# Kernel tuning notes

Measured on AMD Instinct MI355X. Metric: run time of the kernel, lower is better.

Reference implementation:

```python
import jax, jax.numpy as jnp
import numpy as np

D_MODEL = 1024
N_HEADS = 16
HEAD_DIM = D_MODEL // N_HEADS
EPS = 1e-6


def setup_inputs() -> dict:
    key = jax.random.key(0)
    ks = jax.random.split(key, 10)
    s = 0.02
    return {
        "sequence": jax.random.normal(ks[0], (4, 2048, D_MODEL), dtype=jnp.float32),
        "ln_gamma": jnp.ones((D_MODEL,), jnp.float32),
        "ln_beta": jnp.zeros((D_MODEL,), jnp.float32),
        "Wq": jax.random.normal(ks[1], (D_MODEL, D_MODEL), jnp.float32) * s,
        "bq": jnp.zeros((D_MODEL,), jnp.float32),
        "Wk": jax.random.normal(ks[2], (D_MODEL, D_MODEL), jnp.float32) * s,
        "bk": jnp.zeros((D_MODEL,), jnp.float32),
        "Wv": jax.random.normal(ks[3], (D_MODEL, D_MODEL), jnp.float32) * s,
        "bv": jnp.zeros((D_MODEL,), jnp.float32),
        "Wo": jax.random.normal(ks[4], (D_MODEL, D_MODEL), jnp.float32) * s,
        "bo": jnp.zeros((D_MODEL,), jnp.float32),
        "mu": jnp.zeros((1, 1, 1, 1), jnp.float32),
    }


def _split_heads(x):
    b, s, d = x.shape
    return x.reshape(b, s, N_HEADS, HEAD_DIM).transpose(0, 2, 1, 3)  # [B,H,S,hd]


def reference(sequence, ln_gamma, ln_beta, Wq, bq, Wk, bk, Wv, bv, Wo, bo, mu):
    # LayerNorm (eps=1e-6)
    mean = jnp.mean(sequence, axis=-1, keepdims=True)
    var = jnp.mean(jnp.square(sequence - mean), axis=-1, keepdims=True)
    x = (sequence - mean) / jnp.sqrt(var + EPS) * ln_gamma + ln_beta

    # QKV projections (torch Linear: x @ W.T + b)
    q = _split_heads(x @ Wq.T + bq)
    k = _split_heads(x @ Wk.T + bk)
    v = _split_heads(x @ Wv.T + bv)

    scale = HEAD_DIM ** 0.5
    scores = jnp.einsum("bhqd,bhkd->bhqk", q, k) / scale  # [B,H,S,S]
    scores = jax.nn.sigmoid(scores - mu) * jnp.exp(scores)
    scores = scores / jnp.sum(scores, axis=-1, keepdims=True)

    out = jnp.einsum("bhqk,bhkd->bhqd", scores, v)  # [B,H,S,hd]
    b, h, s, hd = out.shape
    out = out.transpose(0, 2, 1, 3).reshape(b, s, h * hd)
    return out @ Wo.T + bo  # dropout is identity at inference
```

## Files before the change

kernel.cpp:

```cpp
#include <hip/hip_runtime.h>
#include <hip/hip_bf16.h>
#include <cstdint>
#include <cstddef>


typedef __bf16 bf16_t;
typedef __bf16 bf16x4 __attribute__((ext_vector_type(4)));
typedef __bf16 bf16x8 __attribute__((ext_vector_type(8)));
typedef float  f32x4  __attribute__((ext_vector_type(4)));
typedef float  f32x16 __attribute__((ext_vector_type(16)));
typedef unsigned u32x4 __attribute__((ext_vector_type(4)));

#define MFMA16(a, b, c) __builtin_amdgcn_mfma_f32_16x16x32_bf16((a), (b), (c), 0, 0, 0)
#define MFMA32(a, b, c) __builtin_amdgcn_mfma_f32_32x32x16_bf16((a), (b), (c), 0, 0, 0)

#if __has_builtin(__builtin_amdgcn_exp2f)
#define VEXP2(x) __builtin_amdgcn_exp2f(x)
#else
#define VEXP2(x) __expf((x) * 0.6931471805599453f)
#endif

__device__ __forceinline__ unsigned cvtpk_bf16(float a, float b) {
  unsigned r;
  asm("v_cvt_pk_bf16_f32 %0, %1, %2" : "=v"(r) : "v"(a), "v"(b));
  return r;
}

__device__ __forceinline__ void plane32_swap(unsigned& a, unsigned& b) {
  asm volatile("v_permlane32_swap_b32 %0, %1" : "+v"(a), "+v"(b));
}

__device__ __forceinline__ void gload16(void* lds, const void* g) {
  __builtin_amdgcn_global_load_lds(
      (__attribute__((address_space(1))) void*)(uintptr_t)g,
      (__attribute__((address_space(3))) void*)(uint32_t)(uintptr_t)lds,
      16, 0, 0);
}

__global__ __launch_bounds__(256) void prep_k(
    const float* __restrict__ s0, const float* __restrict__ s1,
    const float* __restrict__ s2, const float* __restrict__ s3,
    bf16_t* __restrict__ wdst,
    const float* __restrict__ x, const float* __restrict__ gamma,
    const float* __restrict__ beta, bf16_t* __restrict__ xout)
{
  int bid = blockIdx.x;
  int tid = threadIdx.x;
  if (bid < 4096) {
    int part = bid >> 10;
    const float* src = part == 0 ? s0 : part == 1 ? s1 : part == 2 ? s2 : s3;
    int i = (bid & 1023) * 256 + tid;
    float4 v = ((const float4*)src)[i];
    bf16x4 o = { (bf16_t)v.x, (bf16_t)v.y, (bf16_t)v.z, (bf16_t)v.w };
    *(bf16x4*)(wdst + (((size_t)part) << 20) + (size_t)i * 4) = o;
  } else {
    int row = bid - 4096;
    float4 v = ((const float4*)(x + (size_t)row * 1024))[tid];
    float s  = v.x + v.y + v.z + v.w;
    float ss = v.x * v.x + v.y * v.y + v.z * v.z + v.w * v.w;
#pragma unroll
    for (int m = 1; m < 64; m <<= 1) { s += __shfl_xor(s, m); ss += __shfl_xor(ss, m); }
    __shared__ float sh_s[4], sh_q[4];
    int w = tid >> 6;
    if ((tid & 63) == 0) { sh_s[w] = s; sh_q[w] = ss; }
    __syncthreads();
    s  = sh_s[0] + sh_s[1] + sh_s[2] + sh_s[3];
    ss = sh_q[0] + sh_q[1] + sh_q[2] + sh_q[3];
    float mean = s * (1.0f / 1024.0f);
    float var  = ss * (1.0f / 1024.0f) - mean * mean;
    float rstd = rsqrtf(var + 1e-6f);
    float4 gv = ((const float4*)gamma)[tid];
    float4 bv = ((const float4*)beta)[tid];
    bf16x4 o = { (bf16_t)((v.x - mean) * rstd * gv.x + bv.x),
                 (bf16_t)((v.y - mean) * rstd * gv.y + bv.y),
                 (bf16_t)((v.z - mean) * rstd * gv.z + bv.z),
                 (bf16_t)((v.w - mean) * rstd * gv.w + bv.w) };
    *(bf16x4*)(xout + (size_t)row * 1024 + tid * 4) = o;
  }
}

__global__ __launch_bounds__(256) void gemm_bt(
    const bf16_t* __restrict__ A, const bf16_t* __restrict__ Bw,
    const float* __restrict__ b0, const float* __restrict__ b1,
    const float* __restrict__ b2,
    void* __restrict__ o0, void* __restrict__ o1, void* __restrict__ o2,
    int M, int N, int K, int fused)
{
  __shared__ __align__(16) bf16_t a_lds[2][128][32];
  __shared__ __align__(16) bf16_t b_lds[2][128][32];
  const int tid = threadIdx.x;
  const int l = tid & 63, w = tid >> 6;
  const int wr = w >> 1, wc = w & 1;
  const int m0 = blockIdx.y * 128, n0 = blockIdx.x * 128;
  const int lr = l & 15, lg = l >> 4;

  f32x4 acc[4][4] = {};

  const int srow = tid >> 2;
  const int scol = (tid & 3) * 8;
  const bf16_t* ag = A  + (size_t)(m0 + srow) * K + scol;
  const bf16_t* bg = Bw + (size_t)(n0 + srow) * K + scol;

  gload16((char*)a_lds[0] + tid * 16,        ag);
  gload16((char*)a_lds[0] + 4096 + tid * 16, ag + (size_t)64 * K);
  gload16((char*)b_lds[0] + tid * 16,        bg);
  gload16((char*)b_lds[0] + 4096 + tid * 16, bg + (size_t)64 * K);
  __syncthreads();

  int cur = 0;
  for (int k0 = 0; k0 < K; k0 += 32) {
    if (k0 + 32 < K) {
      gload16((char*)a_lds[cur ^ 1] + tid * 16,        ag + k0 + 32);
      gload16((char*)a_lds[cur ^ 1] + 4096 + tid * 16, ag + (size_t)64 * K + k0 + 32);
      gload16((char*)b_lds[cur ^ 1] + tid * 16,        bg + k0 + 32);
      gload16((char*)b_lds[cur ^ 1] + 4096 + tid * 16, bg + (size_t)64 * K + k0 + 32);
    }
    bf16x8 af[4], bf[4];
#pragma unroll
    for (int i = 0; i < 4; ++i) {
      af[i] = *(const bf16x8*)&a_lds[cur][wr * 64 + i * 16 + lr][lg * 8];
      bf[i] = *(const bf16x8*)&b_lds[cur][wc * 64 + i * 16 + lr][lg * 8];
    }
#pragma unroll
    for (int i = 0; i < 4; ++i)
#pragma unroll
      for (int j = 0; j < 4; ++j)
        acc[i][j] = MFMA16(af[i], bf[j], acc[i][j]);
    __syncthreads();
    cur ^= 1;
  }

  int matsel = fused ? (n0 >> 10) : 0;
  const float* bias = matsel == 0 ? b0 : matsel == 1 ? b1 : b2;
  float bs[4];
#pragma unroll
  for (int j = 0; j < 4; ++j) bs[j] = bias[(n0 + wc * 64 + j * 16 + lr) & 1023];

#pragma unroll
  for (int i = 0; i < 4; ++i) {
#pragma unroll
    for (int j = 0; j < 4; ++j) {
      if (fused && matsel == 2) {
        int row0 = m0 + wr * 64 + i * 16 + lg * 4;
        int col  = n0 + wc * 64 + j * 16 + lr;
        int nn = col & 1023;
        int bb = row0 >> 11, s0 = row0 & 2047, hh = nn >> 6, d = nn & 63;
        bf16x4 pv;
#pragma unroll
        for (int r = 0; r < 4; ++r) pv[r] = (bf16_t)(acc[i][j][r] + bs[j]);
        *(bf16x4*)((bf16_t*)o2 + ((((size_t)bb * 16 + hh) * 64) + d) * 2048 + s0) = pv;
      } else {
#pragma unroll
        for (int r = 0; r < 4; ++r) {
          int row = m0 + wr * 64 + i * 16 + lg * 4 + r;
          int col = n0 + wc * 64 + j * 16 + lr;
          float v = acc[i][j][r] + bs[j];
          if (!fused) {
            ((float*)o0)[(size_t)row * N + col] = v;
          } else {
            int nn = col & 1023;
            int bb = row >> 11, s = row & 2047, hh = nn >> 6, d = nn & 63;
            bf16_t* o = matsel ? (bf16_t*)o1 : (bf16_t*)o0;
            if (matsel == 0) v *= 0.18033688011112042f;
            o[((((size_t)bb * 16 + hh) * 2048 + s) << 6) + d] = (bf16_t)v;
          }
        }
      }
    }
  }
}

__global__ __launch_bounds__(512) void attn_k(
    const bf16_t* __restrict__ q, const bf16_t* __restrict__ k,
    const bf16_t* __restrict__ vT, const float* __restrict__ mu_p,
    bf16_t* __restrict__ out)
{
  const int S = 2048;
  int hw = blockIdx.x;
  int vid = (hw & 7) * 64 + (hw >> 3);
  int qt = vid & 7;
  int bh = vid >> 3;
  int h = bh & 15, b = bh >> 4;

  const bf16_t* qb = q  + ((size_t)bh * S + qt * 256) * 64;
  const char* kbase = (const char*)(k  + (size_t)bh * S * 64);
  const char* vbase = (const char*)(vT + (size_t)bh * 64 * S);
  const float emu = __expf(mu_p[0]);

  __shared__ __align__(16) bf16_t k_lds[2][64][64];
  __shared__ __align__(16) bf16_t v_lds[2][64][64];

  const int tid = threadIdx.x, l = tid & 63, w = tid >> 6;
  const int l31 = l & 31, hi = l >> 5;
  const int swzr = (l31 & 7) << 4;

  bf16x8 qf[4];
#pragma unroll
  for (int ch = 0; ch < 4; ++ch)
    qf[ch] = *(const bf16x8*)(qb + (size_t)(w * 32 + l31) * 64 + ch * 16 + hi * 8);

  const int srow = tid >> 3;
  const int ssw  = ((tid & 7) * 16) ^ ((srow & 7) << 4);
  const int koff = srow * 128 + ssw;
  const int voff = srow * 4096 + ssw;

  f32x16 oAcc[2] = {};
  float rs0 = 0.f, rs1 = 0.f;

  gload16((char*)k_lds[0] + tid * 16, kbase + koff);
  gload16((char*)v_lds[0] + tid * 16, vbase + voff);
  __syncthreads();

#pragma unroll 2
  for (int t = 0; t < 32; ++t) {
    const int cur = t & 1;
    if (t + 1 < 32) {
      gload16((char*)k_lds[cur ^ 1] + tid * 16, kbase + koff + (t + 1) * 8192);
      gload16((char*)v_lds[cur ^ 1] + tid * 16, vbase + voff + (t + 1) * 128);
    }

#pragma unroll
    for (int kh = 0; kh < 2; ++kh) {
      f32x16 sc = {};
      __builtin_amdgcn_s_setprio(1);
#pragma unroll
      for (int ch = 0; ch < 4; ++ch) {
        bf16x8 kf = *(const bf16x8*)((const char*)k_lds[cur]
                      + (kh * 32 + l31) * 128 + ((ch * 32 + hi * 16) ^ swzr));
        sc = MFMA32(kf, qf[ch], sc);
      }
      __builtin_amdgcn_s_setprio(0);

      unsigned U[8];
#pragma unroll
      for (int m = 0; m < 8; ++m) {
        float t0 = VEXP2(-sc[2 * m]);
        float t1 = VEXP2(-sc[2 * m + 1]);
        float d0 = fmaf(emu * t0, t0, t0);
        float d1 = fmaf(emu * t1, t1, t1);
        float inv = __builtin_amdgcn_rcpf(d0 * d1);
        float w0 = inv * d1;
        float w1 = inv * d0;
        rs0 += w0; rs1 += w1;
        U[m] = cvtpk_bf16(w0, w1);
      }
      plane32_swap(U[0], U[2]);
      plane32_swap(U[1], U[3]);
      plane32_swap(U[4], U[6]);
      plane32_swap(U[5], U[7]);
      __builtin_amdgcn_s_setprio(1);
#pragma unroll
      for (int cc = 0; cc < 2; ++cc) {
        u32x4 uu = { U[cc * 4 + 0], U[cc * 4 + 1], U[cc * 4 + 2], U[cc * 4 + 3] };
        bf16x8 pa = __builtin_bit_cast(bf16x8, uu);
        int kcol = (kh * 2 + cc) * 32 + hi * 16;
#pragma unroll
        for (int df = 0; df < 2; ++df) {
          bf16x8 vf = *(const bf16x8*)((const char*)v_lds[cur]
                        + (df * 32 + l31) * 128 + (kcol ^ swzr));
          oAcc[df] = MFMA32(pa, vf, oAcc[df]);
        }
      }
      __builtin_amdgcn_s_setprio(0);
    }
    __syncthreads();
  }

  float rs = rs0 + rs1;
  rs += __shfl_xor(rs, 32);
  float rinv = __builtin_amdgcn_rcpf(rs);

#pragma unroll
  for (int r = 0; r < 16; ++r) {
    int q_loc = (r & 3) + 8 * (r >> 2) + 4 * hi;
    float ro = __shfl(rinv, q_loc);
    size_t row = (size_t)b * 2048 + qt * 256 + w * 32 + q_loc;
#pragma unroll
    for (int df = 0; df < 2; ++df) {
      out[row * 1024 + h * 64 + df * 32 + l31] = (bf16_t)(oAcc[df][r] * ro);
    }
  }
}

extern "C" void kernel_launch(void* const* d_in, const int* in_sizes, int n_in,
                              void* d_out, int out_size, void* d_ws, size_t ws_size,
                              hipStream_t stream) {
  const float* seq = (const float*)d_in[0];
  const float* g   = (const float*)d_in[1];
  const float* be  = (const float*)d_in[2];
  const float* Wq  = (const float*)d_in[3];
  const float* bq  = (const float*)d_in[4];
  const float* Wk  = (const float*)d_in[5];
  const float* bk  = (const float*)d_in[6];
  const float* Wv  = (const float*)d_in[7];
  const float* bv  = (const float*)d_in[8];
  const float* Wo  = (const float*)d_in[9];
  const float* bo  = (const float*)d_in[10];
  const float* mu  = (const float*)d_in[11];

  char* ws = (char*)d_ws;
  bf16_t* xb   = (bf16_t*)ws;  ws += (size_t)8192 * 1024 * 2;
  bf16_t* wAll = (bf16_t*)ws;  ws += (size_t)4 * 1024 * 1024 * 2;
  bf16_t* qb   = (bf16_t*)ws;  ws += (size_t)8192 * 1024 * 2;
  bf16_t* kbuf = (bf16_t*)ws;  ws += (size_t)8192 * 1024 * 2;
  bf16_t* vtb  = (bf16_t*)ws;  ws += (size_t)8192 * 1024 * 2;
  bf16_t* ab   = (bf16_t*)ws;  ws += (size_t)8192 * 1024 * 2;
  bf16_t* wqkv = wAll;
  bf16_t* wob  = wAll + (size_t)3 * 1024 * 1024;

  dim3 blk(256);
  prep_k<<<dim3(12288), blk, 0, stream>>>(Wq, Wk, Wv, Wo, wAll, seq, g, be, xb);
  gemm_bt<<<dim3(24, 64), blk, 0, stream>>>(xb, wqkv, bq, bk, bv,
                                            qb, kbuf, vtb, 8192, 3072, 1024, 1);
  attn_k<<<dim3(512), dim3(512), 0, stream>>>(qb, kbuf, vtb, mu, ab);
  gemm_bt<<<dim3(8, 64), blk, 0, stream>>>(ab, wob, bo, nullptr, nullptr,
                                           d_out, nullptr, nullptr, 8192, 1024, 1024, 0);
}
```

Measured before the change: 208.0 us.

## Drop LDS staging in attention; read K/V directly from global with smaller blocks

The attention kernel no longer stages K and V tiles through double-buffered shared memory with barriers. Each wave now loads its MFMA operands straight from global memory (relying on L1/L2 caching), and blocks shrink from 512 to 128 threads covering 64 query rows, with four times as many blocks. This removes the LDS writes, reads and __syncthreads overhead and raises block count for scheduling. In exchange every wave re-reads K/V from cache independently, which multiplies global/L2 traffic, and the vT reads stride 4096 bytes per lane.

```diff
diff --git a/kernel.cpp b/kernel.cpp
--- a/kernel.cpp
+++ b/kernel.cpp
@@ -170,65 +170,48 @@
   }
 }
 
-__global__ __launch_bounds__(512) void attn_k(
+__global__ __launch_bounds__(128) void attn_k(
     const bf16_t* __restrict__ q, const bf16_t* __restrict__ k,
     const bf16_t* __restrict__ vT, const float* __restrict__ mu_p,
     bf16_t* __restrict__ out)
 {
   const int S = 2048;
   int hw = blockIdx.x;
-  int vid = (hw & 7) * 64 + (hw >> 3);
-  int qt = vid & 7;
-  int bh = vid >> 3;
+  int vid = (hw & 7) * 256 + (hw >> 3);
+  int qt = vid & 31;
+  int bh = vid >> 5;
   int h = bh & 15, b = bh >> 4;
 
-  const bf16_t* qb = q  + ((size_t)bh * S + qt * 256) * 64;
-  const char* kbase = (const char*)(k  + (size_t)bh * S * 64);
-  const char* vbase = (const char*)(vT + (size_t)bh * 64 * S);
+  const bf16_t* qb = q + ((size_t)bh * S + qt * 64) * 64;
+  const char* kb = (const char*)(k  + (size_t)bh * S * 64);
+  const char* vb = (const char*)(vT + (size_t)bh * 64 * S);
   const float emu = __expf(mu_p[0]);
-
-  __shared__ __align__(16) bf16_t k_lds[2][64][64];
-  __shared__ __align__(16) bf16_t v_lds[2][64][64];
 
   const int tid = threadIdx.x, l = tid & 63, w = tid >> 6;
   const int l31 = l & 31, hi = l >> 5;
-  const int swzr = (l31 & 7) << 4;
 
   bf16x8 qf[4];
 #pragma unroll
   for (int ch = 0; ch < 4; ++ch)
     qf[ch] = *(const bf16x8*)(qb + (size_t)(w * 32 + l31) * 64 + ch * 16 + hi * 8);
 
-  const int srow = tid >> 3;
-  const int ssw  = ((tid & 7) * 16) ^ ((srow & 7) << 4);
-  const int koff = srow * 128 + ssw;
-  const int voff = srow * 4096 + ssw;
-
   f32x16 oAcc[2] = {};
   float rs0 = 0.f, rs1 = 0.f;
 
-  gload16((char*)k_lds[0] + tid * 16, kbase + koff);
-  gload16((char*)v_lds[0] + tid * 16, vbase + voff);
-  __syncthreads();
-
-#pragma unroll 2
   for (int t = 0; t < 32; ++t) {
-    const int cur = t & 1;
-    if (t + 1 < 32) {
-      gload16((char*)k_lds[cur ^ 1] + tid * 16, kbase + koff + (t + 1) * 8192);
-      gload16((char*)v_lds[cur ^ 1] + tid * 16, vbase + voff + (t + 1) * 128);
-    }
-
 #pragma unroll
     for (int kh = 0; kh < 2; ++kh) {
+      const char* krow = kb + (size_t)(t * 64 + kh * 32 + l31) * 128 + hi * 16;
+      bf16x8 kf0 = *(const bf16x8*)(krow);
+      bf16x8 kf1 = *(const bf16x8*)(krow + 32);
+      bf16x8 kf2 = *(const bf16x8*)(krow + 64);
+      bf16x8 kf3 = *(const bf16x8*)(krow + 96);
       f32x16 sc = {};
       __builtin_amdgcn_s_setprio(1);
-#pragma unroll
-      for (int ch = 0; ch < 4; ++ch) {
-        bf16x8 kf = *(const bf16x8*)((const char*)k_lds[cur]
-                      + (kh * 32 + l31) * 128 + ((ch * 32 + hi * 16) ^ swzr));
-        sc = MFMA32(kf, qf[ch], sc);
-      }
+      sc = MFMA32(kf0, qf[0], sc);
+      sc = MFMA32(kf1, qf[1], sc);
+      sc = MFMA32(kf2, qf[2], sc);
+      sc = MFMA32(kf3, qf[3], sc);
       __builtin_amdgcn_s_setprio(0);
 
       unsigned U[8];
@@ -253,17 +236,15 @@
       for (int cc = 0; cc < 2; ++cc) {
         u32x4 uu = { U[cc * 4 + 0], U[cc * 4 + 1], U[cc * 4 + 2], U[cc * 4 + 3] };
         bf16x8 pa = __builtin_bit_cast(bf16x8, uu);
-        int kcol = (kh * 2 + cc) * 32 + hi * 16;
+        int soff = (t * 64 + (kh * 2 + cc) * 16 + hi * 8) * 2;
 #pragma unroll
         for (int df = 0; df < 2; ++df) {
-          bf16x8 vf = *(const bf16x8*)((const char*)v_lds[cur]
-                        + (df * 32 + l31) * 128 + (kcol ^ swzr));
+          bf16x8 vf = *(const bf16x8*)(vb + (size_t)(df * 32 + l31) * 4096 + soff);
           oAcc[df] = MFMA32(pa, vf, oAcc[df]);
         }
       }
       __builtin_amdgcn_s_setprio(0);
     }
-    __syncthreads();
   }
 
   float rs = rs0 + rs1;
@@ -274,7 +255,7 @@
   for (int r = 0; r < 16; ++r) {
     int q_loc = (r & 3) + 8 * (r >> 2) + 4 * hi;
     float ro = __shfl(rinv, q_loc);
-    size_t row = (size_t)b * 2048 + qt * 256 + w * 32 + q_loc;
+    size_t row = (size_t)b * 2048 + qt * 64 + w * 32 + q_loc;
 #pragma unroll
     for (int df = 0; df < 2; ++df) {
       out[row * 1024 + h * 64 + df * 32 + l31] = (bf16_t)(oAcc[df][r] * ro);
@@ -312,7 +293,7 @@
   prep_k<<<dim3(12288), blk, 0, stream>>>(Wq, Wk, Wv, Wo, wAll, seq, g, be, xb);
   gemm_bt<<<dim3(24, 64), blk, 0, stream>>>(xb, wqkv, bq, bk, bv,
                                             qb, kbuf, vtb, 8192, 3072, 1024, 1);
-  attn_k<<<dim3(512), dim3(512), 0, stream>>>(qb, kbuf, vtb, mu, ab);
+  attn_k<<<dim3(2048), dim3(128), 0, stream>>>(qb, kbuf, vtb, mu, ab);
   gemm_bt<<<dim3(8, 64), blk, 0, stream>>>(ab, wob, bo, nullptr, nullptr,
                                            d_out, nullptr, nullptr, 8192, 1024, 1024, 0);
 }
```

Measured after the change: 387.7 us. 1.86x slower.

## Deepen attention K/V prefetch to 4-stage ring with vmcnt-based waits

Applied to the files above, without the earlier changes.

Replaces the double-buffered K/V LDS pipeline in the attention kernel with a 4-slot ring that keeps two tiles in flight ahead of the current one. Waiting moves from a full __syncthreads to an explicit s_waitcnt vmcnt count plus a single barrier per tile, so global loads overlap more of the compute. LDS use per block doubles to 64 KB, which can lower occupancy. Reusing a slot two tiles later relies on the one barrier per tile to keep it safe.

```diff
diff --git a/kernel.cpp b/kernel.cpp
--- a/kernel.cpp
+++ b/kernel.cpp
@@ -170,6 +170,65 @@
   }
 }
 
+#define ATTN_TILE(T_, ISSUE_, VM_)                                            \
+  {                                                                           \
+    if (ISSUE_) {                                                             \
+      gload16((char*)k_lds[((T_) + 2) & 3] + tid * 16,                        \
+              kbase + koff + ((T_) + 2) * 8192);                              \
+      gload16((char*)v_lds[((T_) + 2) & 3] + tid * 16,                        \
+              vbase + voff + ((T_) + 2) * 128);                               \
+    }                                                                         \
+    asm volatile("s_waitcnt vmcnt(" #VM_ ")" ::: "memory");                   \
+    __builtin_amdgcn_s_barrier();                                             \
+    __builtin_amdgcn_sched_barrier(0);                                        \
+    const char* kldsb_ = (const char*)k_lds[(T_) & 3];                        \
+    const char* vldsb_ = (const char*)v_lds[(T_) & 3];                        \
+    _Pragma("unroll")                                                         \
+    for (int kh = 0; kh < 2; ++kh) {                                          \
+      f32x16 sc = {};                                                         \
+      __builtin_amdgcn_s_setprio(1);                                          \
+      _Pragma("unroll")                                                       \
+      for (int ch = 0; ch < 4; ++ch) {                                        \
+        bf16x8 kf = *(const bf16x8*)(kldsb_ + (kh * 32 + l31) * 128           \
+                                     + ((ch * 32 + hi * 16) ^ swzr));         \
+        sc = MFMA32(kf, qf[ch], sc);                                          \
+      }                                                                       \
+      __builtin_amdgcn_s_setprio(0);                                          \
+      unsigned U[8];                                                          \
+      _Pragma("unroll")                                                       \
+      for (int m = 0; m < 8; ++m) {                                           \
+        float t0 = VEXP2(-sc[2 * m]);                                         \
+        float t1 = VEXP2(-sc[2 * m + 1]);                                     \
+        float d0 = fmaf(emu * t0, t0, t0);                                    \
+        float d1 = fmaf(emu * t1, t1, t1);                                    \
+        float inv = __builtin_amdgcn_rcpf(d0 * d1);                           \
+        float w0 = inv * d1;                                                  \
+        float w1 = inv * d0;                                                  \
+        rs0 += w0; rs1 += w1;                                                 \
+        U[m] = cvtpk_bf16(w0, w1);                                            \
+      }                                                                       \
+      plane32_swap(U[0], U[2]);                                               \
+      plane32_swap(U[1], U[3]);                                               \
+      plane32_swap(U[4], U[6]);                                               \
+      plane32_swap(U[5], U[7]);                                               \
+      __builtin_amdgcn_s_setprio(1);                                          \
+      _Pragma("unroll")                                                       \
+      for (int cc = 0; cc < 2; ++cc) {                                        \
+        u32x4 uu = { U[cc * 4 + 0], U[cc * 4 + 1], U[cc * 4 + 2],             \
+                     U[cc * 4 + 3] };                                         \
+        bf16x8 pa = __builtin_bit_cast(bf16x8, uu);                           \
+        int kcol = (kh * 2 + cc) * 32 + hi * 16;                              \
+        _Pragma("unroll")                                                     \
+        for (int df = 0; df < 2; ++df) {                                      \
+          bf16x8 vf = *(const bf16x8*)(vldsb_ + (df * 32 + l31) * 128         \
+                                       + (kcol ^ swzr));                      \
+          oAcc[df] = MFMA32(pa, vf, oAcc[df]);                                \
+        }                                                                     \
+      }                                                                       \
+      __builtin_amdgcn_s_setprio(0);                                          \
+    }                                                                         \
+  }
+
 __global__ __launch_bounds__(512) void attn_k(
     const bf16_t* __restrict__ q, const bf16_t* __restrict__ k,
     const bf16_t* __restrict__ vT, const float* __restrict__ mu_p,
@@ -187,8 +246,8 @@
   const char* vbase = (const char*)(vT + (size_t)bh * 64 * S);
   const float emu = __expf(mu_p[0]);
 
-  __shared__ __align__(16) bf16_t k_lds[2][64][64];
-  __shared__ __align__(16) bf16_t v_lds[2][64][64];
+  __shared__ __align__(16) bf16_t k_lds[4][64][64];
+  __shared__ __align__(16) bf16_t v_lds[4][64][64];
 
   const int tid = threadIdx.x, l = tid & 63, w = tid >> 6;
   const int l31 = l & 31, hi = l >> 5;
@@ -209,62 +268,15 @@
 
   gload16((char*)k_lds[0] + tid * 16, kbase + koff);
   gload16((char*)v_lds[0] + tid * 16, vbase + voff);
-  __syncthreads();
-
-#pragma unroll 2
-  for (int t = 0; t < 32; ++t) {
-    const int cur = t & 1;
-    if (t + 1 < 32) {
-      gload16((char*)k_lds[cur ^ 1] + tid * 16, kbase + koff + (t + 1) * 8192);
-      gload16((char*)v_lds[cur ^ 1] + tid * 16, vbase + voff + (t + 1) * 128);
-    }
-
-#pragma unroll
-    for (int kh = 0; kh < 2; ++kh) {
-      f32x16 sc = {};
-      __builtin_amdgcn_s_setprio(1);
-#pragma unroll
-      for (int ch = 0; ch < 4; ++ch) {
-        bf16x8 kf = *(const bf16x8*)((const char*)k_lds[cur]
-                      + (kh * 32 + l31) * 128 + ((ch * 32 + hi * 16) ^ swzr));
-        sc = MFMA32(kf, qf[ch], sc);
-      }
-      __builtin_amdgcn_s_setprio(0);
-
-      unsigned U[8];
-#pragma unroll
-      for (int m = 0; m < 8; ++m) {
-        float t0 = VEXP2(-sc[2 * m]);
-        float t1 = VEXP2(-sc[2 * m + 1]);
-        float d0 = fmaf(emu * t0, t0, t0);
-        float d1 = fmaf(emu * t1, t1, t1);
-        float inv = __builtin_amdgcn_rcpf(d0 * d1);
-        float w0 = inv * d1;
-        float w1 = inv * d0;
-        rs0 += w0; rs1 += w1;
-        U[m] = cvtpk_bf16(w0, w1);
-      }
-      plane32_swap(U[0], U[2]);
-      plane32_swap(U[1], U[3]);
-      plane32_swap(U[4], U[6]);
-      plane32_swap(U[5], U[7]);
-      __builtin_amdgcn_s_setprio(1);
-#pragma unroll
-      for (int cc = 0; cc < 2; ++cc) {
-        u32x4 uu = { U[cc * 4 + 0], U[cc * 4 + 1], U[cc * 4 + 2], U[cc * 4 + 3] };
-        bf16x8 pa = __builtin_bit_cast(bf16x8, uu);
-        int kcol = (kh * 2 + cc) * 32 + hi * 16;
-#pragma unroll
-        for (int df = 0; df < 2; ++df) {
-          bf16x8 vf = *(const bf16x8*)((const char*)v_lds[cur]
-                        + (df * 32 + l31) * 128 + (kcol ^ swzr));
-          oAcc[df] = MFMA32(pa, vf, oAcc[df]);
-        }
-      }
-      __builtin_amdgcn_s_setprio(0);
-    }
-    __syncthreads();
-  }
+  gload16((char*)k_lds[1] + tid * 16, kbase + koff + 8192);
+  gload16((char*)v_lds[1] + tid * 16, vbase + voff + 128);
+
+#pragma unroll 4
+  for (int t = 0; t < 28; ++t) ATTN_TILE(t, true, 4);
+  ATTN_TILE(28, true, 4);
+  ATTN_TILE(29, true, 4);
+  ATTN_TILE(30, false, 2);
+  ATTN_TILE(31, false, 0);
 
   float rs = rs0 + rs1;
   rs += __shfl_xor(rs, 32);
```

Result: no change. 207.3 us (-0.3%).
